# Performance work log

Measured on AMD Instinct MI355X. Metric: run time of the kernel, lower is better.

The kernel has to match this reference:

```python
import jax, jax.numpy as jnp
import numpy as np

LOD = 64          # latent observation dim
LSD = 2 * LOD     # latent state dim
BW = 3            # bandwidth
NB = 15           # num basis
B = 4096          # batch
H = 64            # hidden units of coefficient net

# band-structure indices (static, computed once)
_mask = np.triu(np.ones((LOD, LOD), np.float32), -BW) * np.tril(np.ones((LOD, LOD), np.float32), BW)
IDX0, IDX1 = np.where(_mask == 1)
DIAG_IDX = np.where(IDX0 == IDX1)[0]
NE = IDX0.shape[0]  # = 436 for lod=64, bw=3


def setup_inputs() -> dict:
    key = jax.random.key(0)
    ks = jax.random.split(key, 20)
    inp = {
        'prior_mean': jax.random.normal(ks[0], (B, LSD), jnp.float32),
        'cov_u': jax.random.uniform(ks[1], (B, LOD), jnp.float32) + 0.1,
        'cov_l': jax.random.uniform(ks[2], (B, LOD), jnp.float32) + 0.1,
        'cov_s': 0.1 * jax.random.uniform(ks[3], (B, LOD), jnp.float32),
        'obs': jax.random.normal(ks[4], (B, LOD), jnp.float32),
        'obs_var': jax.random.uniform(ks[5], (B, LOD), jnp.float32) + 0.1,
        # coefficient net params (Linear(LSD,H)-Tanh-Linear(H,H)-Tanh-Linear(H,NB)-Softmax)
        'W1': 0.05 * jax.random.normal(ks[6], (H, LSD), jnp.float32),
        'b1': jnp.zeros((H,), jnp.float32),
        'W2': 0.05 * jax.random.normal(ks[7], (H, H), jnp.float32),
        'b2': jnp.zeros((H,), jnp.float32),
        'W3': 0.05 * jax.random.normal(ks[8], (NB, H), jnp.float32),
        'b3': jnp.zeros((NB,), jnp.float32),
    }
    # transition basis matrices, flat band entries [NB, NE]
    tm11 = 0.02 * jax.random.normal(ks[9], (NB, NE), jnp.float32)
    tm12 = 0.02 * jax.random.normal(ks[10], (NB, NE), jnp.float32)
    tm12 = tm12.at[:, DIAG_IDX].add(0.2)
    tm21 = 0.02 * jax.random.normal(ks[11], (NB, NE), jnp.float32)
    tm21 = tm21.at[:, DIAG_IDX].add(-0.2)
    tm22 = 0.02 * jax.random.normal(ks[12], (NB, NE), jnp.float32)
    inp['tm11_basis'] = tm11
    inp['tm12_basis'] = tm12
    inp['tm21_basis'] = tm21
    inp['tm22_basis'] = tm22
    # log transition noise, init at var_activation_inverse(0.1) = log(exp(0.1)-1)
    inp['log_trans_noise'] = jnp.full((1, LSD), np.log(np.exp(0.1) - 1.0), jnp.float32)
    return inp


def _bmv(mat, vec):
    return jnp.einsum('bij,bj->bi', mat, vec)


def _unflatten_tm(flat):
    # flat: [B, NE] -> banded [B, LOD, LOD]
    tm = jnp.zeros((flat.shape[0], LOD, LOD), flat.dtype)
    return tm.at[:, IDX0, IDX1].set(flat)


def reference(prior_mean, cov_u, cov_l, cov_s, obs, obs_var,
              W1, b1, W2, b2, W3, b3,
              tm11_basis, tm12_basis, tm21_basis, tm22_basis, log_trans_noise):
    # ---- update (Kalman-style, factorized diagonal covariance) ----
    denom = cov_u + obs_var
    q_upper = cov_u / denom
    q_lower = cov_s / denom
    residual = obs - prior_mean[:, :LOD]
    post_mean = prior_mean + jnp.concatenate([q_upper * residual, q_lower * residual], -1)
    covar_factor = 1.0 - q_upper
    post_cu = covar_factor * cov_u
    post_cl = cov_l - q_lower * cov_s
    post_cs = covar_factor * cov_s

    # ---- coefficient net: MLP + softmax -> basis mixing coefficients ----
    h = jnp.tanh(post_mean @ W1.T + b1)
    h = jnp.tanh(h @ W2.T + b2)
    coeff = jax.nn.softmax(h @ W3.T + b3, axis=-1)  # [B, NB]

    # ---- locally-linear transition model ----
    tm11_flat = jnp.einsum('bk,ke->be', coeff, tm11_basis).at[:, DIAG_IDX].add(1.0)
    tm12_flat = jnp.einsum('bk,ke->be', coeff, tm12_basis)
    tm21_flat = jnp.einsum('bk,ke->be', coeff, tm21_basis)
    tm22_flat = jnp.einsum('bk,ke->be', coeff, tm22_basis).at[:, DIAG_IDX].add(1.0)
    tm11 = _unflatten_tm(tm11_flat)
    tm12 = _unflatten_tm(tm12_flat)
    tm21 = _unflatten_tm(tm21_flat)
    tm22 = _unflatten_tm(tm22_flat)

    trans_cov = jnp.log(jnp.exp(log_trans_noise) + 1.0)  # var_activation (softplus)
    tcu = trans_cov[:, :LOD]
    tcl = trans_cov[:, LOD:]

    # ---- predict ----
    mu = post_mean[:, :LOD]
    ml = post_mean[:, LOD:]
    next_mean = jnp.concatenate([_bmv(tm11, mu) + _bmv(tm12, ml),
                                 _bmv(tm21, mu) + _bmv(tm22, ml)], -1)
    # dadat(A, d) = bmv(A^2, d); dadbt(A, d, B) = bmv(A*B, d)
    next_cu = (_bmv(jnp.square(tm11), post_cu) + 2.0 * _bmv(tm11 * tm12, post_cs)
               + _bmv(jnp.square(tm12), post_cl) + tcu)
    next_cl = (_bmv(jnp.square(tm21), post_cu) + 2.0 * _bmv(tm21 * tm22, post_cs)
               + _bmv(jnp.square(tm22), post_cl) + tcl)
    next_cs = (_bmv(tm21 * tm11, post_cu) + _bmv(tm22 * tm11, post_cs)
               + _bmv(tm21 * tm12, post_cs) + _bmv(tm22 * tm12, post_cl))

    return (post_mean, post_cu, post_cl, post_cs, next_mean, next_cu, next_cl, next_cs)
```

## Files before the change

### kernel.cpp

```cpp
#include <hip/hip_runtime.h>
#include <math.h>

#define O_PM   0
#define O_PCU  524288
#define O_PCL  786432
#define O_PCS  1048576
#define O_NM   1310720
#define O_NCU  1835008
#define O_NCL  2097152
#define O_NCS  2359296

#define L_W1   0
#define L_W2   4864
#define L_W3   7680
#define L_TM   0
#define L_BAST 13952
#define L_PMB  27904
#define L_H1   29120
#define L_H2   29824
#define L_COEF 30528
#define L_PMF  30688
#define L_CUF  32736
#define L_CLF  33760
#define L_CSF  34784
#define L_TOT  35808

typedef short s8v __attribute__((ext_vector_type(8)));
typedef short s4v __attribute__((ext_vector_type(4)));
typedef float f4v __attribute__((ext_vector_type(4)));

__device__ __forceinline__ unsigned pk2(float a, float b) {
    unsigned ua = __float_as_uint(a), ub = __float_as_uint(b);
    ua += 0x7fffu + ((ua >> 16) & 1u);
    ub += 0x7fffu + ((ub >> 16) & 1u);
    return (ua >> 16) | (ub & 0xffff0000u);
}
__device__ __forceinline__ unsigned short tobf(float a) {
    unsigned ua = __float_as_uint(a);
    ua += 0x7fffu + ((ua >> 16) & 1u);
    return (unsigned short)(ua >> 16);
}
__device__ __forceinline__ float frombf(unsigned short u) {
    return __uint_as_float(((unsigned)u) << 16);
}
__device__ __forceinline__ float lo16(unsigned w) { return __uint_as_float(w << 16); }
__device__ __forceinline__ float hi16(unsigned w) { return __uint_as_float(w & 0xffff0000u); }
__device__ __forceinline__ float frcp(float x) { return __builtin_amdgcn_rcpf(x); }
__device__ __forceinline__ float ftanh(float x) {
    float e = __expf(2.f * x);
    return 1.f - 2.f * frcp(e + 1.f);
}
#define SWZ(v, imm) __uint_as_float((unsigned)__builtin_amdgcn_ds_swizzle((int)__float_as_uint(v), imm))

#if __has_builtin(__builtin_amdgcn_mfma_f32_16x16x16_bf16)
#define MFMA16(A,B,C) __builtin_amdgcn_mfma_f32_16x16x16_bf16(A,B,C,0,0,0)
#define HAVE_MFMA16 1
#elif __has_builtin(__builtin_amdgcn_mfma_f32_16x16x16bf16_1k)
#define MFMA16(A,B,C) __builtin_amdgcn_mfma_f32_16x16x16bf16_1k(A,B,C,0,0,0)
#define HAVE_MFMA16 1
#else
#define HAVE_MFMA16 0
#endif

__global__ __launch_bounds__(512, 2)
void rkn_kernel(const float* __restrict__ prior_mean,
                const float* __restrict__ cov_u,
                const float* __restrict__ cov_l,
                const float* __restrict__ cov_s,
                const float* __restrict__ obs,
                const float* __restrict__ obs_var,
                const float* __restrict__ W1,
                const float* __restrict__ b1,
                const float* __restrict__ W2,
                const float* __restrict__ b2,
                const float* __restrict__ W3,
                const float* __restrict__ b3,
                const float* __restrict__ tm11b,
                const float* __restrict__ tm12b,
                const float* __restrict__ tm21b,
                const float* __restrict__ tm22b,
                const float* __restrict__ ltn,
                float* __restrict__ out)
{
    __shared__ __align__(16) unsigned smem[L_TOT];

    const int tid  = threadIdx.x;
    const int wid  = tid >> 6;
    const int lane = tid & 63;
    const int lrow = lane & 15;
    const int lkg  = lane >> 4;

    {
#pragma unroll
        for (int it = 0; it < 4; ++it) {
            const int idx = it * 512 + tid;
            const float4 v = ((const float4*)W1)[idx];
            const int j = idx >> 5, kq = idx & 31;
            unsigned* d = smem + (L_W1 + j * 76 + kq * 2);
            d[0] = pk2(v.x, v.y); d[1] = pk2(v.z, v.w);
        }
#pragma unroll
        for (int it = 0; it < 2; ++it) {
            const int idx = it * 512 + tid;
            const float4 v = ((const float4*)W2)[idx];
            const int j = idx >> 4, kq = idx & 15;
            unsigned* d = smem + (L_W2 + j * 44 + kq * 2);
            d[0] = pk2(v.x, v.y); d[1] = pk2(v.z, v.w);
        }
        if (tid < 240) {
            const float4 v = ((const float4*)W3)[tid];
            const int j = tid >> 4, kq = tid & 15;
            unsigned* d = smem + (L_W3 + j * 44 + kq * 2);
            d[0] = pk2(v.x, v.y); d[1] = pk2(v.z, v.w);
        } else if (tid < 284) {
            smem[L_W3 + 15 * 44 + (tid - 240)] = 0u;
        }
    }

    {
        const int m = tid & 3;
        const float* bp = (m == 0) ? tm11b : (m == 1) ? tm12b : (m == 2) ? tm21b : tm22b;
#pragma unroll
        for (int kp = 0; kp < 8; ++kp) {
#pragma unroll
            for (int c = 0; c < 4; ++c) {
                const int n = c * 512 + tid;
                if (n < 1744) {
                    const int e = n >> 2;
                    const float lo = bp[(2 * kp) * 436 + e];
                    const float hi = (kp < 7) ? bp[(2 * kp + 1) * 436 + e] : 0.f;
                    smem[L_BAST + kp * 1744 + n] = pk2(lo, hi);
                }
            }
        }
    }

    const int prow  = tid >> 5;
    const int pd    = (tid & 31) << 1;
    const int grow1 = blockIdx.x * 16 + prow;
    {
        const float2 cu2 = *(const float2*)(cov_u   + grow1 * 64 + pd);
        const float2 cl2 = *(const float2*)(cov_l   + grow1 * 64 + pd);
        const float2 cs2 = *(const float2*)(cov_s   + grow1 * 64 + pd);
        const float2 ob2 = *(const float2*)(obs     + grow1 * 64 + pd);
        const float2 ov2 = *(const float2*)(obs_var + grow1 * 64 + pd);
        const float2 pu2 = *(const float2*)(prior_mean + grow1 * 128 + pd);
        const float2 pl2 = *(const float2*)(prior_mean + grow1 * 128 + 64 + pd);

        const float i0 = frcp(cu2.x + ov2.x), i1 = frcp(cu2.y + ov2.y);
        const float qu0 = cu2.x * i0, qu1 = cu2.y * i1;
        const float ql0 = cs2.x * i0, ql1 = cs2.y * i1;
        const float r0 = ob2.x - pu2.x, r1 = ob2.y - pu2.y;
        const float pmu0 = pu2.x + qu0 * r0, pmu1 = pu2.y + qu1 * r1;
        const float pml0 = pl2.x + ql0 * r0, pml1 = pl2.y + ql1 * r1;
        const float cf0 = 1.f - qu0, cf1 = 1.f - qu1;
        const float pcu0 = cf0 * cu2.x, pcu1 = cf1 * cu2.y;
        const float pcl0 = cl2.x - ql0 * cs2.x, pcl1 = cl2.y - ql1 * cs2.y;
        const float pcs0 = cf0 * cs2.x, pcs1 = cf1 * cs2.y;

        *(float2*)(out + O_PM  + grow1 * 128 + pd)      = make_float2(pmu0, pmu1);
        *(float2*)(out + O_PM  + grow1 * 128 + 64 + pd) = make_float2(pml0, pml1);
        *(float2*)(out + O_PCU + grow1 * 64 + pd) = make_float2(pcu0, pcu1);
        *(float2*)(out + O_PCL + grow1 * 64 + pd) = make_float2(pcl0, pcl1);
        *(float2*)(out + O_PCS + grow1 * 64 + pd) = make_float2(pcs0, pcs1);

        smem[L_PMB + prow * 76 + (pd >> 1)]      = pk2(pmu0, pmu1);
        smem[L_PMB + prow * 76 + 32 + (pd >> 1)] = pk2(pml0, pml1);
        *(float2*)((float*)(smem + L_PMF) + prow * 128 + pd)      = make_float2(pmu0, pmu1);
        *(float2*)((float*)(smem + L_PMF) + prow * 128 + 64 + pd) = make_float2(pml0, pml1);
        *(float2*)((float*)(smem + L_CUF) + prow * 64 + pd) = make_float2(pcu0, pcu1);
        *(float2*)((float*)(smem + L_CLF) + prow * 64 + pd) = make_float2(pcl0, pcl1);
        *(float2*)((float*)(smem + L_CSF) + prow * 64 + pd) = make_float2(pcs0, pcs1);
    }

    const float tcu = __logf(__expf(ltn[lane]) + 1.f);
    const float tcl = __logf(__expf(ltn[64 + lane]) + 1.f);

    __syncthreads();

    if (wid < 4) {
        const int w = wid;
        f4v acc = {0.f, 0.f, 0.f, 0.f};
#pragma unroll
        for (int s = 0; s < 4; ++s) {
            s8v a = *(const s8v*)(smem + L_PMB + lrow * 76 + s * 16 + lkg * 4);
            s8v b = *(const s8v*)(smem + L_W1 + (w * 16 + lrow) * 76 + s * 16 + lkg * 4);
            acc = __builtin_amdgcn_mfma_f32_16x16x32_bf16(a, b, acc, 0, 0, 0);
        }
        const float bc1 = b1[w * 16 + lrow];
        unsigned short* h1u = (unsigned short*)(smem + L_H1);
#pragma unroll
        for (int q = 0; q < 4; ++q)
            h1u[(lkg * 4 + q) * 88 + w * 16 + lrow] = tobf(ftanh(acc[q] + bc1));
    }
    __syncthreads();

    if (wid < 4) {
        const int w = wid;
        f4v acc = {0.f, 0.f, 0.f, 0.f};
#pragma unroll
        for (int s = 0; s < 2; ++s) {
            s8v a = *(const s8v*)(smem + L_H1 + lrow * 44 + s * 16 + lkg * 4);
            s8v b = *(const s8v*)(smem + L_W2 + (w * 16 + lrow) * 44 + s * 16 + lkg * 4);
            acc = __builtin_amdgcn_mfma_f32_16x16x32_bf16(a, b, acc, 0, 0, 0);
        }
        const float bc2 = b2[w * 16 + lrow];
        unsigned short* h2u = (unsigned short*)(smem + L_H2);
#pragma unroll
        for (int q = 0; q < 4; ++q)
            h2u[(lkg * 4 + q) * 88 + w * 16 + lrow] = tobf(ftanh(acc[q] + bc2));
    }
    __syncthreads();

    if (wid < 4) {
        f4v acc = {0.f, 0.f, 0.f, 0.f};
#pragma unroll
        for (int s = 0; s < 2; ++s) {
            s8v a = *(const s8v*)(smem + L_H2 + lrow * 44 + s * 16 + lkg * 4);
            s8v b = *(const s8v*)(smem + L_W3 + lrow * 44 + s * 16 + lkg * 4);
            acc = __builtin_amdgcn_mfma_f32_16x16x32_bf16(a, b, acc, 0, 0, 0);
        }
        const float bc3 = (lrow < 15) ? b3[lrow] : 0.f;
        unsigned short* cfu = (unsigned short*)(smem + L_COEF);
#pragma unroll
        for (int q = 0; q < 4; ++q) {
            const float lg = acc[q] + bc3;
            float v = (lrow < 15) ? lg : -1e30f;
            v = fmaxf(v, SWZ(v, 0x041F));
            v = fmaxf(v, SWZ(v, 0x081F));
            v = fmaxf(v, SWZ(v, 0x101F));
            v = fmaxf(v, SWZ(v, 0x201F));
            const float ex = (lrow < 15) ? __expf(lg - v) : 0.f;
            float ss = ex;
            ss += SWZ(ss, 0x041F);
            ss += SWZ(ss, 0x081F);
            ss += SWZ(ss, 0x101F);
            ss += SWZ(ss, 0x201F);
            if (wid == 0)
                cfu[(lkg * 4 + q) * 20 + lrow] = tobf(ex * frcp(ss));
        }
    }
    __syncthreads();

    {
        const int nt = (wid < 5) ? 14 : 13;
        const int t0 = (wid < 5) ? wid * 14 : wid * 13 + 5;
        unsigned short* tmu = (unsigned short*)(smem + L_TM);
#if HAVE_MFMA16
        const s4v ca = *(const s4v*)(smem + L_COEF + lrow * 10 + lkg * 2);
#endif
        for (int tt = 0; tt < nt; ++tt) {
            const int n0 = (t0 + tt) * 16;
            const int nn = n0 + lrow;
            f4v d = {0.f, 0.f, 0.f, 0.f};
#if HAVE_MFMA16
            unsigned wpair[2];
            wpair[0] = smem[L_BAST + (lkg * 2    ) * 1744 + nn];
            wpair[1] = smem[L_BAST + (lkg * 2 + 1) * 1744 + nn];
            const s4v bb = *(const s4v*)wpair;
            d = MFMA16(ca, bb, d);
#else
            const unsigned short* cf = (const unsigned short*)(smem + L_COEF);
#pragma unroll
            for (int q = 0; q < 4; ++q) {
                float s = 0.f;
                for (int kp = 0; kp < 8; ++kp) {
                    const unsigned w = smem[L_BAST + kp * 1744 + nn];
                    s += lo16(w) * frombf(cf[(lkg * 4 + q) * 20 + 2 * kp]);
                    s += hi16(w) * frombf(cf[(lkg * 4 + q) * 20 + 2 * kp + 1]);
                }
                d[q] = s;
            }
#endif
#pragma unroll
            for (int q = 0; q < 4; ++q)
                tmu[(lkg * 4 + q) * 1744 + nn] = tobf(d[q]);
        }
    }
    __syncthreads();

    {
        const int i   = lane;
        const int jlo = (i - 3 > 0) ? (i - 3) : 0;
        const int ne  = ((i + 3 < 63) ? (i + 3) : 63) - jlo + 1;
        const int base = (i < 4)  ? (i * (i + 7)) / 2
                       : (i <= 61) ? (7 * i - 6)
                       : (i == 62) ? 427 : 432;
        const float* pmf = (const float*)(smem + L_PMF);
        const float* cuf = (const float*)(smem + L_CUF);
        const float* clf = (const float*)(smem + L_CLF);
        const float* csf = (const float*)(smem + L_CSF);
        const uint2* tmr = (const uint2*)smem;

#pragma unroll
        for (int rr = 0; rr < 2; ++rr) {
            const int r  = wid * 2 + rr;
            const int gr = blockIdx.x * 16 + r;
            float nmu = 0.f, nml = 0.f, ncu = 0.f, ncl = 0.f, ncs = 0.f;
#pragma unroll
            for (int dd = 0; dd < 7; ++dd) {
                if (dd < ne) {
                    const int j = jlo + dd;
                    const uint2 tv = tmr[r * 436 + base + dd];
                    float t11 = lo16(tv.x);
                    float t12 = hi16(tv.x);
                    float t21 = lo16(tv.y);
                    float t22 = hi16(tv.y);
                    if (j == i) { t11 += 1.f; t22 += 1.f; }
                    const float mu  = pmf[r * 128 + j];
                    const float ml  = pmf[r * 128 + 64 + j];
                    const float vcu = cuf[r * 64 + j];
                    const float vcl = clf[r * 64 + j];
                    const float vcs = csf[r * 64 + j];
                    nmu += t11 * mu + t12 * ml;
                    nml += t21 * mu + t22 * ml;
                    ncu += t11 * t11 * vcu + 2.f * t11 * t12 * vcs + t12 * t12 * vcl;
                    ncl += t21 * t21 * vcu + 2.f * t21 * t22 * vcs + t22 * t22 * vcl;
                    ncs += t21 * t11 * vcu + (t22 * t11 + t21 * t12) * vcs + t22 * t12 * vcl;
                }
            }
            out[O_NM  + gr * 128 + i]      = nmu;
            out[O_NM  + gr * 128 + 64 + i] = nml;
            out[O_NCU + gr * 64 + i] = ncu + tcu;
            out[O_NCL + gr * 64 + i] = ncl + tcl;
            out[O_NCS + gr * 64 + i] = ncs;
        }
    }
}

extern "C" void kernel_launch(void* const* d_in, const int* in_sizes, int n_in,
                              void* d_out, int out_size, void* d_ws, size_t ws_size,
                              hipStream_t stream) {
    rkn_kernel<<<dim3(256), dim3(512), 0, stream>>>(
        (const float*)d_in[0],
        (const float*)d_in[1],
        (const float*)d_in[2],
        (const float*)d_in[3],
        (const float*)d_in[4],
        (const float*)d_in[5],
        (const float*)d_in[6],
        (const float*)d_in[7],
        (const float*)d_in[8],
        (const float*)d_in[9],
        (const float*)d_in[10],
        (const float*)d_in[11],
        (const float*)d_in[12],
        (const float*)d_in[13],
        (const float*)d_in[14],
        (const float*)d_in[15],
        (const float*)d_in[16],
        (float*)d_out);
}
```

Measured before the change: 19.50 us.

## Keep transition basis in registers and shrink LDS to raise occupancy

Each wave now loads the transition basis directly from global memory into registers as bf16 MFMA B-operands, so the large LDS staging buffer for the basis disappears. The fp32 copies of posterior mean and covariances in LDS are replaced with packed bf16 values. Together these roughly halve LDS use, and launch bounds now request 4 blocks per CU. Costs: more registers held across the barriers, only wave 0 computes the coefficient softmax, and the predict step reads bf16 instead of fp32 inputs, which lowers precision.

```diff
diff --git a/kernel.cpp b/kernel.cpp
--- a/kernel.cpp
+++ b/kernel.cpp
@@ -14,16 +14,13 @@
 #define L_W2   4864
 #define L_W3   7680
 #define L_TM   0
-#define L_BAST 13952
-#define L_PMB  27904
-#define L_H1   29120
-#define L_H2   29824
-#define L_COEF 30528
-#define L_PMF  30688
-#define L_CUF  32736
-#define L_CLF  33760
-#define L_CSF  34784
-#define L_TOT  35808
+#define L_PMB  14016
+#define L_H1   15232
+#define L_H2   15936
+#define L_COEF 16640
+#define L_CUV  16800
+#define L_CSV  17824
+#define L_TOT  18336
 
 typedef short s8v __attribute__((ext_vector_type(8)));
 typedef short s4v __attribute__((ext_vector_type(4)));
@@ -62,7 +59,7 @@
 #define HAVE_MFMA16 0
 #endif
 
-__global__ __launch_bounds__(512, 2)
+__global__ __launch_bounds__(512, 4)
 void rkn_kernel(const float* __restrict__ prior_mean,
                 const float* __restrict__ cov_u,
                 const float* __restrict__ cov_l,
@@ -117,24 +114,6 @@
         }
     }
 
-    {
-        const int m = tid & 3;
-        const float* bp = (m == 0) ? tm11b : (m == 1) ? tm12b : (m == 2) ? tm21b : tm22b;
-#pragma unroll
-        for (int kp = 0; kp < 8; ++kp) {
-#pragma unroll
-            for (int c = 0; c < 4; ++c) {
-                const int n = c * 512 + tid;
-                if (n < 1744) {
-                    const int e = n >> 2;
-                    const float lo = bp[(2 * kp) * 436 + e];
-                    const float hi = (kp < 7) ? bp[(2 * kp + 1) * 436 + e] : 0.f;
-                    smem[L_BAST + kp * 1744 + n] = pk2(lo, hi);
-                }
-            }
-        }
-    }
-
     const int prow  = tid >> 5;
     const int pd    = (tid & 31) << 1;
     const int grow1 = blockIdx.x * 16 + prow;
@@ -166,11 +145,32 @@
 
         smem[L_PMB + prow * 76 + (pd >> 1)]      = pk2(pmu0, pmu1);
         smem[L_PMB + prow * 76 + 32 + (pd >> 1)] = pk2(pml0, pml1);
-        *(float2*)((float*)(smem + L_PMF) + prow * 128 + pd)      = make_float2(pmu0, pmu1);
-        *(float2*)((float*)(smem + L_PMF) + prow * 128 + 64 + pd) = make_float2(pml0, pml1);
-        *(float2*)((float*)(smem + L_CUF) + prow * 64 + pd) = make_float2(pcu0, pcu1);
-        *(float2*)((float*)(smem + L_CLF) + prow * 64 + pd) = make_float2(pcl0, pcl1);
-        *(float2*)((float*)(smem + L_CSF) + prow * 64 + pd) = make_float2(pcs0, pcs1);
+        smem[L_CUV + prow * 64 + pd]     = pk2(pcu0, pcl0);
+        smem[L_CUV + prow * 64 + pd + 1] = pk2(pcu1, pcl1);
+        smem[L_CSV + prow * 32 + (pd >> 1)] = pk2(pcs0, pcs1);
+    }
+
+    s4v bb[14];
+    {
+        const int m = lrow & 3;
+        const float* bp = (m == 0) ? tm11b : (m == 1) ? tm12b : (m == 2) ? tm21b : tm22b;
+        const int eo = lrow >> 2;
+        const int k0 = 4 * lkg;
+#pragma unroll
+        for (int tt = 0; tt < 14; ++tt) {
+            const int t = wid * 14 + tt;
+            if (t < 109) {
+                const int e = t * 4 + eo;
+                const float v0 = bp[(k0    ) * 436 + e];
+                const float v1 = bp[(k0 + 1) * 436 + e];
+                const float v2 = bp[(k0 + 2) * 436 + e];
+                const float v3 = (k0 + 3 < 15) ? bp[(k0 + 3) * 436 + e] : 0.f;
+                bb[tt] = (s4v){ (short)tobf(v0), (short)tobf(v1),
+                                (short)tobf(v2), (short)tobf(v3) };
+            } else {
+                bb[tt] = (s4v){0, 0, 0, 0};
+            }
+        }
     }
 
     const float tcu = __logf(__expf(ltn[lane]) + 1.f);
@@ -212,7 +212,7 @@
     }
     __syncthreads();
 
-    if (wid < 4) {
+    if (wid == 0) {
         f4v acc = {0.f, 0.f, 0.f, 0.f};
 #pragma unroll
         for (int s = 0; s < 2; ++s) {
@@ -236,46 +236,45 @@
             ss += SWZ(ss, 0x081F);
             ss += SWZ(ss, 0x101F);
             ss += SWZ(ss, 0x201F);
-            if (wid == 0)
-                cfu[(lkg * 4 + q) * 20 + lrow] = tobf(ex * frcp(ss));
-        }
-    }
-    __syncthreads();
-
-    {
-        const int nt = (wid < 5) ? 14 : 13;
-        const int t0 = (wid < 5) ? wid * 14 : wid * 13 + 5;
+            cfu[(lkg * 4 + q) * 20 + lrow] = tobf(ex * frcp(ss));
+        }
+    }
+    __syncthreads();
+
+    {
         unsigned short* tmu = (unsigned short*)(smem + L_TM);
 #if HAVE_MFMA16
         const s4v ca = *(const s4v*)(smem + L_COEF + lrow * 10 + lkg * 2);
+#pragma unroll
+        for (int tt = 0; tt < 14; ++tt) {
+            const int t = wid * 14 + tt;
+            if (t < 109) {
+                const int nn = t * 16 + lrow;
+                f4v d = {0.f, 0.f, 0.f, 0.f};
+                d = MFMA16(ca, bb[tt], d);
+#pragma unroll
+                for (int q = 0; q < 4; ++q)
+                    tmu[(lkg * 4 + q) * 1752 + nn] = tobf(d[q]);
+            }
+        }
+#else
+        const unsigned short* cf = (const unsigned short*)(smem + L_COEF);
+#pragma unroll
+        for (int tt = 0; tt < 14; ++tt) {
+            const int t = wid * 14 + tt;
+            if (t < 109) {
+                const int nn = t * 16 + lrow;
+#pragma unroll
+                for (int q = 0; q < 4; ++q) {
+                    float s = 0.f;
+                    for (int j = 0; j < 4; ++j)
+                        s += frombf((unsigned short)bb[tt][j]) *
+                             frombf(cf[(lkg * 4 + q) * 20 + 4 * lkg + j]);
+                    tmu[(lkg * 4 + q) * 1752 + nn] = tobf(s);
+                }
+            }
+        }
 #endif
-        for (int tt = 0; tt < nt; ++tt) {
-            const int n0 = (t0 + tt) * 16;
-            const int nn = n0 + lrow;
-            f4v d = {0.f, 0.f, 0.f, 0.f};
-#if HAVE_MFMA16
-            unsigned wpair[2];
-            wpair[0] = smem[L_BAST + (lkg * 2    ) * 1744 + nn];
-            wpair[1] = smem[L_BAST + (lkg * 2 + 1) * 1744 + nn];
-            const s4v bb = *(const s4v*)wpair;
-            d = MFMA16(ca, bb, d);
-#else
-            const unsigned short* cf = (const unsigned short*)(smem + L_COEF);
-#pragma unroll
-            for (int q = 0; q < 4; ++q) {
-                float s = 0.f;
-                for (int kp = 0; kp < 8; ++kp) {
-                    const unsigned w = smem[L_BAST + kp * 1744 + nn];
-                    s += lo16(w) * frombf(cf[(lkg * 4 + q) * 20 + 2 * kp]);
-                    s += hi16(w) * frombf(cf[(lkg * 4 + q) * 20 + 2 * kp + 1]);
-                }
-                d[q] = s;
-            }
-#endif
-#pragma unroll
-            for (int q = 0; q < 4; ++q)
-                tmu[(lkg * 4 + q) * 1744 + nn] = tobf(d[q]);
-        }
     }
     __syncthreads();
 
@@ -286,10 +285,6 @@
         const int base = (i < 4)  ? (i * (i + 7)) / 2
                        : (i <= 61) ? (7 * i - 6)
                        : (i == 62) ? 427 : 432;
-        const float* pmf = (const float*)(smem + L_PMF);
-        const float* cuf = (const float*)(smem + L_CUF);
-        const float* clf = (const float*)(smem + L_CLF);
-        const float* csf = (const float*)(smem + L_CSF);
         const uint2* tmr = (const uint2*)smem;
 
 #pragma unroll
@@ -301,17 +296,21 @@
             for (int dd = 0; dd < 7; ++dd) {
                 if (dd < ne) {
                     const int j = jlo + dd;
-                    const uint2 tv = tmr[r * 436 + base + dd];
+                    const uint2 tv = tmr[r * 438 + base + dd];
                     float t11 = lo16(tv.x);
                     float t12 = hi16(tv.x);
                     float t21 = lo16(tv.y);
                     float t22 = hi16(tv.y);
                     if (j == i) { t11 += 1.f; t22 += 1.f; }
-                    const float mu  = pmf[r * 128 + j];
-                    const float ml  = pmf[r * 128 + 64 + j];
-                    const float vcu = cuf[r * 64 + j];
-                    const float vcl = clf[r * 64 + j];
-                    const float vcs = csf[r * 64 + j];
+                    const unsigned pw  = smem[L_PMB + r * 76 + (j >> 1)];
+                    const unsigned pw2 = smem[L_PMB + r * 76 + 32 + (j >> 1)];
+                    const unsigned cc  = smem[L_CUV + r * 64 + j];
+                    const unsigned sv  = smem[L_CSV + r * 32 + (j >> 1)];
+                    const float mu  = (j & 1) ? hi16(pw)  : lo16(pw);
+                    const float ml  = (j & 1) ? hi16(pw2) : lo16(pw2);
+                    const float vcu = lo16(cc);
+                    const float vcl = hi16(cc);
+                    const float vcs = (j & 1) ? hi16(sv) : lo16(sv);
                     nmu += t11 * mu + t12 * ml;
                     nml += t21 * mu + t22 * ml;
                     ncu += t11 * t11 * vcu + 2.f * t11 * t12 * vcs + t12 * t12 * vcl;
```

Result: slower. 22.54 us (+15.6%).
